# Kernel tuning notes

Measured on AMD Instinct MI355X. Metric: run time of the kernel, lower is better.

Reference implementation:

```python
import jax, jax.numpy as jnp
import numpy as np

DEPTH = 8          # complete binary tree: 2^8-1 = 255 internal nodes, 256 leaves
N_FEAT = 32
N_CLASSES = 10
BATCH = 131072


def setup_inputs() -> dict:
    key = jax.random.key(0)
    k_x, k_t, k_f, k_c = jax.random.split(key, 4)
    n_internal = (1 << DEPTH) - 1
    n_leaves = 1 << DEPTH
    x = jax.random.normal(k_x, (BATCH, N_FEAT), dtype=jnp.float32)
    # learnable per-node thresholds (initialized from the sklearn tree's thresholds)
    thresholds = jax.random.normal(k_t, (n_internal,), dtype=jnp.float32) * 0.5
    # non-differentiable split feature index per internal node
    feats = jax.random.randint(k_f, (n_internal,), 0, N_FEAT, dtype=jnp.int32)
    # majority class per leaf (argmax of sklearn value array)
    leaf_class = jax.random.randint(k_c, (n_leaves,), 0, N_CLASSES, dtype=jnp.int32)
    return {"x": x, "thresholds": thresholds, "feats": feats, "leaf_class": leaf_class}


def reference(x, thresholds, feats, leaf_class):
    # Soft decision-tree traversal. Internal nodes stored in level (heap) order:
    # level d occupies indices [2^d - 1, 2^(d+1) - 1). Children of the j-th node
    # of a level are the (2j)-th and (2j+1)-th nodes of the next level, so an
    # interleaved stack+reshape reproduces the heap child ordering exactly.
    B = x.shape[0]
    probs = jnp.ones((B, 1), dtype=x.dtype)  # root path probability
    start = 0
    for d in range(DEPTH):
        n = 1 << d
        f = feats[start:start + n]               # [n] split feature per node
        t = thresholds[start:start + n]          # [n] learnable threshold
        act = jax.nn.sigmoid(x[:, f] - t[None, :])   # [B, n] right-branch gate
        # left child gets (1 - act), right child gets act (matches _split_approx)
        probs = jnp.stack([probs * (1.0 - act), probs * act], axis=-1).reshape(B, 2 * n)
        start += n
    # sum leaf path probabilities per majority class (stack + sum in original)
    onehot = jax.nn.one_hot(leaf_class, N_CLASSES, dtype=x.dtype)  # [n_leaves, C]
    p = probs @ onehot                                             # [B, C]
    return p
```

## Files before the change

### kernel.cpp

```cpp
#include <hip/hip_runtime.h>


#define NFEAT 32
#define NCLS  10
#define TPB   256
#define RPB   128
#define L2E   1.4426950408889634f

__device__ __forceinline__ float fexp2(float z) {
#if __has_builtin(__builtin_amdgcn_exp2f)
  return __builtin_amdgcn_exp2f(z);
#else
  return exp2f(z);
#endif
}
__device__ __forceinline__ float frcp(float z) {
#if __has_builtin(__builtin_amdgcn_rcpf)
  return __builtin_amdgcn_rcpf(z);
#else
  return 1.0f / z;
#endif
}

__device__ __forceinline__ void evaln(const int2* nd, const float* xT,
                                      int n, int row, float p,
                                      float& pl, float& pr) {
  const int2 r = nd[n];
  const float x2 = xT[(r.y << 7) + row];
  const float e = fexp2(__int_as_float(r.x) - x2);
  const float a = frcp(1.0f + e);
  pr = p * a;
  pl = pr * e;
}

template <int D>
__device__ __forceinline__ void dfs(const int2* nd, const int4* nd7,
                                    const float* xT, float* accA, float* accB,
                                    int n, int t, int row, float p) {
  if constexpr (D == 7) {
    const int4 r = nd7[n - 127];
    const float x2 = xT[(r.y << 7) + row];
    const float e = fexp2(__int_as_float(r.x) - x2);
    const float a = frcp(1.0f + e);
    const float pr = p * a;
    const float pl = pr * e;
    accA[(r.z << 8) + t] += pl;
    accB[(r.w << 8) + t] += pr;
  } else {
    float pl, pr;
    evaln(nd, xT, n, row, p, pl, pr);
    dfs<D + 1>(nd, nd7, xT, accA, accB, 2 * n + 1, t, row, pl);
    dfs<D + 1>(nd, nd7, xT, accA, accB, 2 * n + 2, t, row, pr);
  }
}

__global__ __launch_bounds__(TPB, 4)
void dt_kernel(const float* __restrict__ x,
               const float* __restrict__ thr,
               const int*   __restrict__ feats,
               const int*   __restrict__ leafc,
               float*       __restrict__ out) {
  __shared__ int2  s_nd[127];
  __shared__ int4  s_nd7[128];
  __shared__ float s_xT[NFEAT * RPB];
  __shared__ float s_accA[NCLS * TPB];
  __shared__ float s_accB[NCLS * TPB];

  const int t   = threadIdx.x;
  const int row = t & (RPB - 1);
  const int h   = t >> 7;

  if (t < 127) {
    s_nd[t] = make_int2(__float_as_int(thr[t] * L2E), feats[t]);
  } else if (t < 255) {
    const int n7 = t - 127;
    s_nd7[n7] = make_int4(__float_as_int(thr[t] * L2E), feats[t],
                          leafc[2 * n7], leafc[2 * n7 + 1]);
  }

  const float4* xg = (const float4*)x + (size_t)blockIdx.x * (RPB * NFEAT / 4);
#pragma unroll
  for (int k = 0; k < 4; ++k) {
    const int i4 = k * TPB + t;
    const float4 v = xg[i4];
    const int r  = i4 >> 3;
    const int c0 = (i4 & 7) * 4;
    s_xT[(c0 + 0) * RPB + r] = v.x * L2E;
    s_xT[(c0 + 1) * RPB + r] = v.y * L2E;
    s_xT[(c0 + 2) * RPB + r] = v.z * L2E;
    s_xT[(c0 + 3) * RPB + r] = v.w * L2E;
  }

#pragma unroll
  for (int k = 0; k < NCLS; ++k) {
    s_accA[k * TPB + t] = 0.0f;
    s_accB[k * TPB + t] = 0.0f;
  }

  __syncthreads();

  float pl, pr;
  evaln(s_nd, s_xT, 0, row, 1.0f, pl, pr);
  const float pd1 = h ? pr : pl;
  evaln(s_nd, s_xT, 1 + h, row, pd1, pl, pr);
  const float pA = pl, pB = pr;
  float pm0, pm1, pm2, pm3;
  evaln(s_nd, s_xT, 3 + 2 * h, row, pA, pm0, pm1);
  evaln(s_nd, s_xT, 4 + 2 * h, row, pB, pm2, pm3);

  const int mb = 7 + 4 * h;
#pragma unroll 1
  for (int s = 0; s < 4; ++s) {
    const float p = (s == 0) ? pm0 : (s == 1) ? pm1 : (s == 2) ? pm2 : pm3;
    dfs<3>(s_nd, s_nd7, s_xT, s_accA, s_accB, mb + s, t, row, p);
  }

  __syncthreads();

  float* og = out + (size_t)blockIdx.x * (RPB * NCLS);
#pragma unroll
  for (int k = 0; k < 5; ++k) {
    const int j = k * TPB + t;
    const int r = j / NCLS;
    const int c = j - r * NCLS;
    og[j] = (s_accA[(c << 8) + r] + s_accA[(c << 8) + RPB + r]) +
            (s_accB[(c << 8) + r] + s_accB[(c << 8) + RPB + r]);
  }
}

extern "C" void kernel_launch(void* const* d_in, const int* in_sizes, int n_in,
                              void* d_out, int out_size, void* d_ws, size_t ws_size,
                              hipStream_t stream) {
  const float* x     = (const float*)d_in[0];
  const float* thr   = (const float*)d_in[1];
  const int*   feats = (const int*)d_in[2];
  const int*   leafc = (const int*)d_in[3];
  float*       out   = (float*)d_out;

  const int B    = in_sizes[0] / NFEAT;
  const int grid = B / RPB;

  dt_kernel<<<grid, TPB, 0, stream>>>(x, thr, feats, leafc, out);
}
```

Measured before the change: 85.86 us.

## Split each row's tree across four threads and accumulate with shared atomics

Rows per block drop from 128 to 64, so four threads share each row and each thread walks only two depth-3 subtrees instead of four. The two per-thread class accumulator arrays are replaced by one shared per-row array updated with unsafeAtomicAdd, and launch bounds now request 8 blocks per CU. This halves per-thread serial work and shrinks LDS per block so more blocks can be resident. In exchange it adds LDS atomic contention among the four threads of a row, plus redundant evaluation of the top tree levels. A leftover empty loop is harmless dead code.

After: 241.4 us. 181% more time.

```diff
diff --git a/kernel.cpp b/kernel.cpp
--- a/kernel.cpp
+++ b/kernel.cpp
@@ -4,7 +4,7 @@
 #define NFEAT 32
 #define NCLS  10
 #define TPB   256
-#define RPB   128
+#define RPB   64
 #define L2E   1.4426950408889634f
 
 __device__ __forceinline__ float fexp2(float z) {
@@ -26,7 +26,7 @@
                                       int n, int row, float p,
                                       float& pl, float& pr) {
   const int2 r = nd[n];
-  const float x2 = xT[(r.y << 7) + row];
+  const float x2 = xT[(r.y << 6) + row];
   const float e = fexp2(__int_as_float(r.x) - x2);
   const float a = frcp(1.0f + e);
   pr = p * a;
@@ -35,26 +35,26 @@
 
 template <int D>
 __device__ __forceinline__ void dfs(const int2* nd, const int4* nd7,
-                                    const float* xT, float* accA, float* accB,
-                                    int n, int t, int row, float p) {
+                                    const float* xT, float* acc,
+                                    int n, int row, float p) {
   if constexpr (D == 7) {
     const int4 r = nd7[n - 127];
-    const float x2 = xT[(r.y << 7) + row];
+    const float x2 = xT[(r.y << 6) + row];
     const float e = fexp2(__int_as_float(r.x) - x2);
     const float a = frcp(1.0f + e);
     const float pr = p * a;
     const float pl = pr * e;
-    accA[(r.z << 8) + t] += pl;
-    accB[(r.w << 8) + t] += pr;
+    unsafeAtomicAdd(&acc[(r.z << 6) + row], pl);
+    unsafeAtomicAdd(&acc[(r.w << 6) + row], pr);
   } else {
     float pl, pr;
     evaln(nd, xT, n, row, p, pl, pr);
-    dfs<D + 1>(nd, nd7, xT, accA, accB, 2 * n + 1, t, row, pl);
-    dfs<D + 1>(nd, nd7, xT, accA, accB, 2 * n + 2, t, row, pr);
+    dfs<D + 1>(nd, nd7, xT, acc, 2 * n + 1, row, pl);
+    dfs<D + 1>(nd, nd7, xT, acc, 2 * n + 2, row, pr);
   }
 }
 
-__global__ __launch_bounds__(TPB, 4)
+__global__ __launch_bounds__(TPB, 8)
 void dt_kernel(const float* __restrict__ x,
                const float* __restrict__ thr,
                const int*   __restrict__ feats,
@@ -63,12 +63,11 @@
   __shared__ int2  s_nd[127];
   __shared__ int4  s_nd7[128];
   __shared__ float s_xT[NFEAT * RPB];
-  __shared__ float s_accA[NCLS * TPB];
-  __shared__ float s_accB[NCLS * TPB];
+  __shared__ float s_acc[NCLS * RPB];
 
   const int t   = threadIdx.x;
   const int row = t & (RPB - 1);
-  const int h   = t >> 7;
+  const int h   = t >> 6;
 
   if (t < 127) {
     s_nd[t] = make_int2(__float_as_int(thr[t] * L2E), feats[t]);
@@ -80,7 +79,7 @@
 
   const float4* xg = (const float4*)x + (size_t)blockIdx.x * (RPB * NFEAT / 4);
 #pragma unroll
-  for (int k = 0; k < 4; ++k) {
+  for (int k = 0; k < 2; ++k) {
     const int i4 = k * TPB + t;
     const float4 v = xg[i4];
     const int r  = i4 >> 3;
@@ -92,39 +91,41 @@
   }
 
 #pragma unroll
-  for (int k = 0; k < NCLS; ++k) {
-    s_accA[k * TPB + t] = 0.0f;
-    s_accB[k * TPB + t] = 0.0f;
+  for (int k = 0; k < NCLS; ++k)
+    if (k * TPB + t < NCLS * RPB) ;
+#pragma unroll
+  for (int k = 0; k < NCLS * RPB / TPB + 1; ++k) {
+    const int j = k * TPB + t;
+    if (j < NCLS * RPB) s_acc[j] = 0.0f;
   }
 
   __syncthreads();
 
   float pl, pr;
   evaln(s_nd, s_xT, 0, row, 1.0f, pl, pr);
-  const float pd1 = h ? pr : pl;
-  evaln(s_nd, s_xT, 1 + h, row, pd1, pl, pr);
-  const float pA = pl, pB = pr;
-  float pm0, pm1, pm2, pm3;
-  evaln(s_nd, s_xT, 3 + 2 * h, row, pA, pm0, pm1);
-  evaln(s_nd, s_xT, 4 + 2 * h, row, pB, pm2, pm3);
+  const float pd1 = (h >> 1) ? pr : pl;
+  evaln(s_nd, s_xT, 1 + (h >> 1), row, pd1, pl, pr);
+  const float pd2 = (h & 1) ? pr : pl;
+  evaln(s_nd, s_xT, 3 + h, row, pd2, pl, pr);
 
-  const int mb = 7 + 4 * h;
+  const int mb = 7 + 2 * h;
+  const float ps0 = pl, ps1 = pr;
 #pragma unroll 1
-  for (int s = 0; s < 4; ++s) {
-    const float p = (s == 0) ? pm0 : (s == 1) ? pm1 : (s == 2) ? pm2 : pm3;
-    dfs<3>(s_nd, s_nd7, s_xT, s_accA, s_accB, mb + s, t, row, p);
+  for (int s = 0; s < 2; ++s) {
+    dfs<3>(s_nd, s_nd7, s_xT, s_acc, mb + s, row, s ? ps1 : ps0);
   }
 
   __syncthreads();
 
   float* og = out + (size_t)blockIdx.x * (RPB * NCLS);
 #pragma unroll
-  for (int k = 0; k < 5; ++k) {
+  for (int k = 0; k < 3; ++k) {
     const int j = k * TPB + t;
-    const int r = j / NCLS;
-    const int c = j - r * NCLS;
-    og[j] = (s_accA[(c << 8) + r] + s_accA[(c << 8) + RPB + r]) +
-            (s_accB[(c << 8) + r] + s_accB[(c << 8) + RPB + r]);
+    if (j < RPB * NCLS) {
+      const int r = j / NCLS;
+      const int c = j - r * NCLS;
+      og[j] = s_acc[(c << 6) + r];
+    }
   }
 }
 
```
